# Performance work log

Measured on AMD Instinct MI355X. Metric: run time of the kernel, lower is better.

The kernel has to match this reference:

```python
import jax, jax.numpy as jnp
import numpy as np

N, DIM, TOPK = 8192, 512, 10


def setup_inputs() -> dict:
    key = jax.random.key(0)
    k1, k2, k3, k4, k5 = jax.random.split(key, 5)
    s = DIM ** -0.5
    return {
        "X": jax.random.normal(k1, (N, DIM), dtype=jnp.float32),
        "Wh": jax.random.normal(k2, (DIM, DIM), dtype=jnp.float32) * s,
        "bh": jax.random.normal(k3, (DIM,), dtype=jnp.float32) * s,
        "Wt": jax.random.normal(k4, (DIM, DIM), dtype=jnp.float32) * s,
        "bt": jax.random.normal(k5, (DIM,), dtype=jnp.float32) * s,
    }


def reference(X, Wh, bh, Wt, bt):
    n, dim = X.shape
    scale = dim ** -0.5
    e_h = X @ Wh.T + bh                      # [n, dim]
    e_t = X @ Wt.T + bt                      # [n, dim]
    logits = (e_h @ e_t.T) * scale           # [n, n]
    topk_val, topk_idx = jax.lax.top_k(logits, TOPK)   # [n, k]
    weights = jax.nn.softmax(topk_val, axis=-1)        # [n, k]
    src = jnp.repeat(jnp.arange(n, dtype=jnp.int32), TOPK)  # [n*k]
    dst = topk_idx.reshape(-1).astype(jnp.int32)
    edge_index = jnp.stack([src, dst], axis=0)          # [2, n*k]
    edge_weight = weights.reshape(-1)                   # [n*k]
    return edge_index, edge_weight
```

## Files before the change

### kernel.cpp

```cpp
#include <hip/hip_runtime.h>
#include <math.h>

#define NROWS 8192
#define DIMK  512
#define TOPK  10
#define SCALE 0.044194173824159223f

#define ETM 128
#define ETN 64
#define ETK 32
#define NTHREADS 256

#define BM 128
#define BN 128
#define BK 32
#define NS2 16
#define SCOLS2 (NROWS / NS2)
#define NQ 256
#define CAP 64
#define TMARGIN 2.0f

typedef __attribute__((ext_vector_type(8))) short bf16x8;
typedef __attribute__((ext_vector_type(4))) float f32x4;

__device__ __forceinline__ unsigned short f2bf(float f) {
  unsigned int u = __float_as_uint(f);
  u = (u + 0x7FFF + ((u >> 16) & 1)) >> 16;
  return (unsigned short)u;
}

__device__ __forceinline__ void gld16(const void* g, const void* lds) {
  __builtin_amdgcn_global_load_lds(
      (const __attribute__((address_space(1))) void*)g,
      (__attribute__((address_space(3))) void*)lds, 16, 0, 0);
}

__global__ __launch_bounds__(NTHREADS, 3)
void embed_gemm(const float* __restrict__ X,
                const float* __restrict__ Wh, const float* __restrict__ bh,
                const float* __restrict__ Wt, const float* __restrict__ bt,
                float* __restrict__ Eh, float* __restrict__ Et,
                unsigned short* __restrict__ Ehb, unsigned short* __restrict__ Etb) {
  __shared__ float As[2][ETK][ETM + 4];
  __shared__ float Bs[2][ETK][ETN + 4];

  const int tid = threadIdx.x;
  const int rowBase = blockIdx.x * ETM;
  const int colBase = blockIdx.y * ETN;
  const float* W  = (colBase < DIMK) ? Wh : Wt;
  const float* bb = (colBase < DIMK) ? bh : bt;
  float* Out            = (colBase < DIMK) ? Eh : Et;
  unsigned short* Outb  = (colBase < DIMK) ? Ehb : Etb;
  const int colOff = colBase & (DIMK - 1);

  const int tx = tid & 15, ty = tid >> 4;
  float acc[8][4];
#pragma unroll
  for (int r = 0; r < 8; ++r)
#pragma unroll
    for (int c = 0; c < 4; ++c) acc[r][c] = 0.f;

  auto stage = [&](int buf, int kt) {
#pragma unroll
    for (int u = 0; u < 4; ++u) {
      const int idx = tid + u * NTHREADS;
      const int r = idx >> 3;
      const int dc = idx & 7;
      const float4 av = *(const float4*)&X[(size_t)(rowBase + r) * DIMK + kt + dc * 4];
      As[buf][dc * 4 + 0][r] = av.x; As[buf][dc * 4 + 1][r] = av.y;
      As[buf][dc * 4 + 2][r] = av.z; As[buf][dc * 4 + 3][r] = av.w;
    }
#pragma unroll
    for (int u = 0; u < 2; ++u) {
      const int idx = tid + u * NTHREADS;
      const int r = idx >> 3;
      const int dc = idx & 7;
      const float4 bv = *(const float4*)&W[(size_t)(colOff + r) * DIMK + kt + dc * 4];
      Bs[buf][dc * 4 + 0][r] = bv.x; Bs[buf][dc * 4 + 1][r] = bv.y;
      Bs[buf][dc * 4 + 2][r] = bv.z; Bs[buf][dc * 4 + 3][r] = bv.w;
    }
  };
  auto compute = [&](int buf) {
#pragma unroll 4
    for (int k = 0; k < ETK; ++k) {
      const float4 a0 = *(const float4*)&As[buf][k][ty * 4];
      const float4 a1 = *(const float4*)&As[buf][k][64 + ty * 4];
      const float4 b  = *(const float4*)&Bs[buf][k][tx * 4];
      const float ar[8] = {a0.x, a0.y, a0.z, a0.w, a1.x, a1.y, a1.z, a1.w};
      const float br[4] = {b.x, b.y, b.z, b.w};
#pragma unroll
      for (int r = 0; r < 8; ++r)
#pragma unroll
        for (int c = 0; c < 4; ++c)
          acc[r][c] = fmaf(ar[r], br[c], acc[r][c]);
    }
  };

  stage(0, 0);
  __syncthreads();
#pragma unroll 1
  for (int ki = 0; ki < DIMK / ETK; ki += 2) {
    if (ki + 1 < DIMK / ETK) stage(1, (ki + 1) * ETK);
    compute(0);
    __syncthreads();
    if (ki + 2 < DIMK / ETK) stage(0, (ki + 2) * ETK);
    compute(1);
    __syncthreads();
  }

  const float4 bv = *(const float4*)&bb[colOff + tx * 4];
  const float br[4] = {bv.x, bv.y, bv.z, bv.w};
#pragma unroll
  for (int r = 0; r < 8; ++r) {
    const int row = rowBase + ((r < 4) ? (ty * 4 + r) : (64 + ty * 4 + r - 4));
    float4 o;
    o.x = acc[r][0] + br[0]; o.y = acc[r][1] + br[1];
    o.z = acc[r][2] + br[2]; o.w = acc[r][3] + br[3];
    const size_t off = (size_t)row * DIMK + colOff + tx * 4;
    *(float4*)&Out[off] = o;
    ushort4 ob;
    ob.x = f2bf(o.x); ob.y = f2bf(o.y); ob.z = f2bf(o.z); ob.w = f2bf(o.w);
    *(ushort4*)&Outb[off] = ob;
  }
}

__global__ __launch_bounds__(256, 3)
void screen_store(const unsigned short* __restrict__ Ehb,
                  const unsigned short* __restrict__ Etb,
                  float* __restrict__ tmax, unsigned short* __restrict__ Sc) {
  __shared__ unsigned short As[2][BM * BK];
  __shared__ unsigned short Bs[2][BN * BK];
  __shared__ unsigned short Csb[BM * 72];

  const int tid = threadIdx.x;
  const int rowBase = blockIdx.x * BM;
  const int strip = blockIdx.y;
  const int w = tid >> 6, lane = tid & 63;
  const int q = lane >> 4, l15 = lane & 15;
  const int wr = (w & 1) * 64, wc = (w >> 1) * 64;
  const int rr = tid >> 1, hq = tid & 1;

  const int c0 = tid, c1 = tid + 256;
  const int wb0 = __builtin_amdgcn_readfirstlane(tid & ~63);
  const int wb1 = wb0 + 256;
  const int ar0 = c0 >> 2, ac0 = (c0 & 3) * 8;
  const int ar1 = c1 >> 2, ac1 = (c1 & 3) * 8;

  for (int ct = 0; ct < SCOLS2; ct += BN) {
    const int colBase = strip * SCOLS2 + ct;
    const int tileG = colBase >> 7;
    f32x4 acc[4][4];
#pragma unroll
    for (int i = 0; i < 4; ++i)
#pragma unroll
      for (int j = 0; j < 4; ++j) acc[i][j] = (f32x4){0.f, 0.f, 0.f, 0.f};

    auto stage = [&](int buf, int kt) {
      gld16(Ehb + (size_t)(rowBase + ar0) * DIMK + kt + ac0, As[buf] + wb0 * 8);
      gld16(Ehb + (size_t)(rowBase + ar1) * DIMK + kt + ac1, As[buf] + wb1 * 8);
      gld16(Etb + (size_t)(colBase + ar0) * DIMK + kt + ac0, Bs[buf] + wb0 * 8);
      gld16(Etb + (size_t)(colBase + ar1) * DIMK + kt + ac1, Bs[buf] + wb1 * 8);
    };
    auto compute = [&](int buf) {
      bf16x8 af[4], bf[4];
#pragma unroll
      for (int i = 0; i < 4; ++i)
        af[i] = *(const bf16x8*)&As[buf][(wr + i * 16 + l15) * BK + q * 8];
#pragma unroll
      for (int j = 0; j < 4; ++j)
        bf[j] = *(const bf16x8*)&Bs[buf][(wc + j * 16 + l15) * BK + q * 8];
#pragma unroll
      for (int i = 0; i < 4; ++i)
#pragma unroll
        for (int j = 0; j < 4; ++j)
          acc[i][j] = __builtin_amdgcn_mfma_f32_16x16x32_bf16(af[i], bf[j], acc[i][j], 0, 0, 0);
    };

    stage(0, 0);
    __syncthreads();
#pragma unroll 1
    for (int ki = 0; ki < DIMK / BK; ki += 2) {
      if (ki + 1 < DIMK / BK) stage(1, (ki + 1) * BK);
      compute(0);
      __syncthreads();
      if (ki + 2 < DIMK / BK) stage(0, (ki + 2) * BK);
      compute(1);
      __syncthreads();
    }

#pragma unroll
    for (int half = 0; half < 2; ++half) {
      if ((w >> 1) == half) {
#pragma unroll
        for (int i = 0; i < 4; ++i)
#pragma unroll
          for (int j = 0; j < 4; ++j)
#pragma unroll
            for (int rg = 0; rg < 4; ++rg)
              Csb[(wr + i * 16 + q * 4 + rg) * 72 + j * 16 + l15] = f2bf(acc[i][j][rg]);
      }
      __syncthreads();
      float m = -INFINITY;
      uint4 buf4[4];
#pragma unroll
      for (int k = 0; k < 4; ++k) {
        buf4[k] = *(const uint4*)&Csb[rr * 72 + hq * 32 + k * 8];
        const unsigned int uu[4] = {buf4[k].x, buf4[k].y, buf4[k].z, buf4[k].w};
#pragma unroll
        for (int e = 0; e < 4; ++e) {
          m = fmaxf(m, __uint_as_float(uu[e] << 16));
          m = fmaxf(m, __uint_as_float(uu[e] & 0xFFFF0000u));
        }
      }
      tmax[(size_t)(rowBase + rr) * NQ + tileG * 4 + half * 2 + hq] = m;
      uint4* dst = (uint4*)&Sc[(size_t)(rowBase + rr) * NROWS + colBase + half * 64 + hq * 32];
#pragma unroll
      for (int k = 0; k < 4; ++k) dst[k] = buf4[k];
      __syncthreads();
    }
  }
}

__global__ __launch_bounds__(256)
void collect_rescore(const unsigned short* __restrict__ Sc,
                     const float* __restrict__ tmax,
                     const float* __restrict__ Eh, const float* __restrict__ Et,
                     float* __restrict__ out) {
  __shared__ int lcnt[4];
  __shared__ int lcand[4][CAP];
  const int lane = threadIdx.x & 63;
  const int wid = threadIdx.x >> 6;
  const int r = blockIdx.x * 4 + wid;

  if (lane == 0) lcnt[wid] = 0;
  __syncthreads();

  const f32x4 gm = *(const f32x4*)&tmax[(size_t)r * NQ + lane * 4];
  float a0 = gm[0], a1 = gm[1], a2 = gm[2], a3 = gm[3];
  float g = -INFINITY;
#pragma unroll 1
  for (int j = 0; j < TOPK; ++j) {
    const float lm = fmaxf(fmaxf(a0, a1), fmaxf(a2, a3));
    g = lm;
#pragma unroll
    for (int off = 32; off > 0; off >>= 1) g = fmaxf(g, __shfl_xor(g, off, 64));
    const unsigned long long ball = __ballot(lm == g);
    const int src = __ffsll((long long)ball) - 1;
    if (lane == src) {
      if      (a0 == g) a0 = -INFINITY;
      else if (a1 == g) a1 = -INFINITY;
      else if (a2 == g) a2 = -INFINITY;
      else              a3 = -INFINITY;
    }
  }
  const float tt = g - TMARGIN;

  const unsigned short* row = Sc + (size_t)r * NROWS;
#pragma unroll 1
  for (int it = 0; it < NROWS / 512; ++it) {
    const int cc0 = it * 512 + lane * 8;
    const uint4 u = *(const uint4*)&row[cc0];
    const unsigned int uu[4] = {u.x, u.y, u.z, u.w};
#pragma unroll
    for (int e = 0; e < 4; ++e) {
      const float lo = __uint_as_float(uu[e] << 16);
      const float hi = __uint_as_float(uu[e] & 0xFFFF0000u);
      if (lo >= tt) {
        const int p = atomicAdd(&lcnt[wid], 1);
        if (p < CAP) lcand[wid][p] = cc0 + 2 * e;
      }
      if (hi >= tt) {
        const int p = atomicAdd(&lcnt[wid], 1);
        if (p < CAP) lcand[wid][p] = cc0 + 2 * e + 1;
      }
    }
  }
  __syncthreads();

  const int n = min(lcnt[wid], CAP);
  const bool active = lane < n;
  const int col = active ? lcand[wid][lane] : 0;

  const float* a = Eh + (size_t)r * DIMK;
  const float* b = Et + (size_t)col * DIMK;
  float p = 0.f;
#pragma unroll 4
  for (int k = 0; k < DIMK; k += 4) {
    const float4 av = *(const float4*)&a[k];
    const float4 bv = *(const float4*)&b[k];
    p = fmaf(av.x, bv.x, p);
    p = fmaf(av.y, bv.y, p);
    p = fmaf(av.z, bv.z, p);
    p = fmaf(av.w, bv.w, p);
  }
  float v = active ? p * SCALE : -INFINITY;
  const int vc = active ? col : 0x7FFFFFFF;

  float myv = -INFINITY; int myc = 0; float m = 0.f;
  float vv = v; int cc2 = vc;
#pragma unroll 1
  for (int j = 0; j < TOPK; ++j) {
    float bvv = vv; int bcc = cc2;
#pragma unroll
    for (int off = 32; off > 0; off >>= 1) {
      const float ov = __shfl_xor(bvv, off, 64);
      const int oc = __shfl_xor(bcc, off, 64);
      if (ov > bvv || (ov == bvv && oc < bcc)) { bvv = ov; bcc = oc; }
    }
    if (j == 0) m = bvv;
    if (lane == j) { myv = bvv; myc = bcc; }
    if (vv == bvv && cc2 == bcc) vv = -INFINITY;
  }

  float sum = 0.f;
#pragma unroll
  for (int j = 0; j < TOPK; ++j) sum += expf(__shfl(myv, j, 64) - m);
  const float inv = 1.0f / sum;

  if (lane < TOPK) {
    const size_t ro = (size_t)r * TOPK + lane;
    out[ro] = (float)r;
    out[(size_t)NROWS * TOPK + ro] = (float)myc;
    out[2 * (size_t)NROWS * TOPK + ro] = expf(myv - m) * inv;
  }
}

extern "C" void kernel_launch(void* const* d_in, const int* in_sizes, int n_in,
                              void* d_out, int out_size, void* d_ws, size_t ws_size,
                              hipStream_t stream) {
  const float* X  = (const float*)d_in[0];
  const float* Wh = (const float*)d_in[1];
  const float* bh = (const float*)d_in[2];
  const float* Wt = (const float*)d_in[3];
  const float* bt = (const float*)d_in[4];
  float* out = (float*)d_out;

  char* ws = (char*)d_ws;
  const size_t embB  = (size_t)NROWS * DIMK * sizeof(float);
  const size_t embBH = (size_t)NROWS * DIMK * sizeof(unsigned short);
  const size_t tmaxB = (size_t)NROWS * NQ * sizeof(float);
  float* Eh   = (float*)ws;
  float* Et   = (float*)(ws + embB);
  unsigned short* Ehb = (unsigned short*)(ws + 2 * embB);
  unsigned short* Etb = (unsigned short*)(ws + 2 * embB + embBH);
  float* tmax = (float*)(ws + 2 * embB + 2 * embBH);
  unsigned short* Sc = (unsigned short*)(ws + 2 * embB + 2 * embBH + tmaxB);

  dim3 blk(NTHREADS);
  dim3 g1(NROWS / ETM, (2 * DIMK) / ETN);
  embed_gemm<<<g1, blk, 0, stream>>>(X, Wh, bh, Wt, bt, Eh, Et, Ehb, Etb);

  dim3 g2(NROWS / BM, NS2);
  screen_store<<<g2, blk, 0, stream>>>(Ehb, Etb, tmax, Sc);

  collect_rescore<<<NROWS / 4, blk, 0, stream>>>(Sc, tmax, Eh, Et, out);
}
```

Baseline: 417.5 us.

## Widen embed GEMM tile with packed FMA and split candidate scan across waves

```diff
diff --git a/kernel.cpp b/kernel.cpp
--- a/kernel.cpp
+++ b/kernel.cpp
@@ -7,7 +7,7 @@
 #define SCALE 0.044194173824159223f
 
 #define ETM 128
-#define ETN 64
+#define ETN 128
 #define ETK 32
 #define NTHREADS 256
 
@@ -22,6 +22,7 @@
 
 typedef __attribute__((ext_vector_type(8))) short bf16x8;
 typedef __attribute__((ext_vector_type(4))) float f32x4;
+typedef __attribute__((ext_vector_type(2))) float f32x2;
 
 __device__ __forceinline__ unsigned short f2bf(float f) {
   unsigned int u = __float_as_uint(f);
@@ -35,7 +36,16 @@
       (__attribute__((address_space(3))) void*)lds, 16, 0, 0);
 }
 
-__global__ __launch_bounds__(NTHREADS, 3)
+__device__ __forceinline__ f32x2 pk_fma(f32x2 a, f32x2 b, f32x2 c) {
+#if __has_builtin(__builtin_elementwise_fma)
+  return __builtin_elementwise_fma(a, b, c);
+#else
+  f32x2 r; r[0] = fmaf(a[0], b[0], c[0]); r[1] = fmaf(a[1], b[1], c[1]);
+  return r;
+#endif
+}
+
+__global__ __launch_bounds__(NTHREADS, 2)
 void embed_gemm(const float* __restrict__ X,
                 const float* __restrict__ Wh, const float* __restrict__ bh,
                 const float* __restrict__ Wt, const float* __restrict__ bt,
@@ -54,11 +64,11 @@
   const int colOff = colBase & (DIMK - 1);
 
   const int tx = tid & 15, ty = tid >> 4;
-  float acc[8][4];
+  f32x2 acc2[8][4];
 #pragma unroll
   for (int r = 0; r < 8; ++r)
 #pragma unroll
-    for (int c = 0; c < 4; ++c) acc[r][c] = 0.f;
+    for (int p = 0; p < 4; ++p) acc2[r][p] = (f32x2){0.f, 0.f};
 
   auto stage = [&](int buf, int kt) {
 #pragma unroll
@@ -71,7 +81,7 @@
       As[buf][dc * 4 + 2][r] = av.z; As[buf][dc * 4 + 3][r] = av.w;
     }
 #pragma unroll
-    for (int u = 0; u < 2; ++u) {
+    for (int u = 0; u < 4; ++u) {
       const int idx = tid + u * NTHREADS;
       const int r = idx >> 3;
       const int dc = idx & 7;
@@ -85,14 +95,18 @@
     for (int k = 0; k < ETK; ++k) {
       const float4 a0 = *(const float4*)&As[buf][k][ty * 4];
       const float4 a1 = *(const float4*)&As[buf][k][64 + ty * 4];
-      const float4 b  = *(const float4*)&Bs[buf][k][tx * 4];
+      const float4 b0 = *(const float4*)&Bs[buf][k][tx * 4];
+      const float4 b1 = *(const float4*)&Bs[buf][k][64 + tx * 4];
       const float ar[8] = {a0.x, a0.y, a0.z, a0.w, a1.x, a1.y, a1.z, a1.w};
-      const float br[4] = {b.x, b.y, b.z, b.w};
-#pragma unroll
-      for (int r = 0; r < 8; ++r)
-#pragma unroll
-        for (int c = 0; c < 4; ++c)
-          acc[r][c] = fmaf(ar[r], br[c], acc[r][c]);
+      const f32x2 bp[4] = {(f32x2){b0.x, b0.y}, (f32x2){b0.z, b0.w},
+                           (f32x2){b1.x, b1.y}, (f32x2){b1.z, b1.w}};
+#pragma unroll
+      for (int r = 0; r < 8; ++r) {
+        const f32x2 ar2 = (f32x2){ar[r], ar[r]};
+#pragma unroll
+        for (int p = 0; p < 4; ++p)
+          acc2[r][p] = pk_fma(ar2, bp[p], acc2[r][p]);
+      }
     }
   };
 
@@ -108,19 +122,30 @@
     __syncthreads();
   }
 
-  const float4 bv = *(const float4*)&bb[colOff + tx * 4];
-  const float br[4] = {bv.x, bv.y, bv.z, bv.w};
+  float br[8];
+  {
+    const float4 bv0 = *(const float4*)&bb[colOff + tx * 4];
+    const float4 bv1 = *(const float4*)&bb[colOff + 64 + tx * 4];
+    br[0] = bv0.x; br[1] = bv0.y; br[2] = bv0.z; br[3] = bv0.w;
+    br[4] = bv1.x; br[5] = bv1.y; br[6] = bv1.z; br[7] = bv1.w;
+  }
 #pragma unroll
   for (int r = 0; r < 8; ++r) {
     const int row = rowBase + ((r < 4) ? (ty * 4 + r) : (64 + ty * 4 + r - 4));
-    float4 o;
-    o.x = acc[r][0] + br[0]; o.y = acc[r][1] + br[1];
-    o.z = acc[r][2] + br[2]; o.w = acc[r][3] + br[3];
-    const size_t off = (size_t)row * DIMK + colOff + tx * 4;
-    *(float4*)&Out[off] = o;
-    ushort4 ob;
-    ob.x = f2bf(o.x); ob.y = f2bf(o.y); ob.z = f2bf(o.z); ob.w = f2bf(o.w);
-    *(ushort4*)&Outb[off] = ob;
+    float4 o0, o1;
+    o0.x = acc2[r][0][0] + br[0]; o0.y = acc2[r][0][1] + br[1];
+    o0.z = acc2[r][1][0] + br[2]; o0.w = acc2[r][1][1] + br[3];
+    o1.x = acc2[r][2][0] + br[4]; o1.y = acc2[r][2][1] + br[5];
+    o1.z = acc2[r][3][0] + br[6]; o1.w = acc2[r][3][1] + br[7];
+    const size_t off0 = (size_t)row * DIMK + colOff + tx * 4;
+    const size_t off1 = off0 + 64;
+    *(float4*)&Out[off0] = o0;
+    *(float4*)&Out[off1] = o1;
+    ushort4 q0, q1;
+    q0.x = f2bf(o0.x); q0.y = f2bf(o0.y); q0.z = f2bf(o0.z); q0.w = f2bf(o0.w);
+    q1.x = f2bf(o1.x); q1.y = f2bf(o1.y); q1.z = f2bf(o1.z); q1.w = f2bf(o1.w);
+    *(ushort4*)&Outb[off0] = q0;
+    *(ushort4*)&Outb[off1] = q1;
   }
 }
 
@@ -226,13 +251,13 @@
                      const float* __restrict__ tmax,
                      const float* __restrict__ Eh, const float* __restrict__ Et,
                      float* __restrict__ out) {
-  __shared__ int lcnt[4];
-  __shared__ int lcand[4][CAP];
+  __shared__ int lcnt;
+  __shared__ int lcand[CAP];
   const int lane = threadIdx.x & 63;
   const int wid = threadIdx.x >> 6;
-  const int r = blockIdx.x * 4 + wid;
-
-  if (lane == 0) lcnt[wid] = 0;
+  const int r = blockIdx.x;
+
+  if (threadIdx.x == 0) lcnt = 0;
   __syncthreads();
 
   const f32x4 gm = *(const f32x4*)&tmax[(size_t)r * NQ + lane * 4];
@@ -257,8 +282,8 @@
 
   const unsigned short* row = Sc + (size_t)r * NROWS;
 #pragma unroll 1
-  for (int it = 0; it < NROWS / 512; ++it) {
-    const int cc0 = it * 512 + lane * 8;
+  for (int it = 0; it < 4; ++it) {
+    const int cc0 = (wid * 4 + it) * 512 + lane * 8;
     const uint4 u = *(const uint4*)&row[cc0];
     const unsigned int uu[4] = {u.x, u.y, u.z, u.w};
 #pragma unroll
@@ -266,20 +291,21 @@
       const float lo = __uint_as_float(uu[e] << 16);
       const float hi = __uint_as_float(uu[e] & 0xFFFF0000u);
       if (lo >= tt) {
-        const int p = atomicAdd(&lcnt[wid], 1);
-        if (p < CAP) lcand[wid][p] = cc0 + 2 * e;
+        const int p = atomicAdd(&lcnt, 1);
+        if (p < CAP) lcand[p] = cc0 + 2 * e;
       }
       if (hi >= tt) {
-        const int p = atomicAdd(&lcnt[wid], 1);
-        if (p < CAP) lcand[wid][p] = cc0 + 2 * e + 1;
+        const int p = atomicAdd(&lcnt, 1);
+        if (p < CAP) lcand[p] = cc0 + 2 * e + 1;
       }
     }
   }
   __syncthreads();
-
-  const int n = min(lcnt[wid], CAP);
+  if (wid != 0) return;
+
+  const int n = min(lcnt, CAP);
   const bool active = lane < n;
-  const int col = active ? lcand[wid][lane] : 0;
+  const int col = active ? lcand[lane] : 0;
 
   const float* a = Eh + (size_t)r * DIMK;
   const float* b = Et + (size_t)col * DIMK;
@@ -353,5 +379,5 @@
   dim3 g2(NROWS / BM, NS2);
   screen_store<<<g2, blk, 0, stream>>>(Ehb, Etb, tmax, Sc);
 
-  collect_rescore<<<NROWS / 4, blk, 0, stream>>>(Sc, tmax, Eh, Et, out);
-}
+  collect_rescore<<<NROWS, blk, 0, stream>>>(Sc, tmax, Eh, Et, out);
+}
```

Measured after the change: 381.6 us. -8.6%, faster.
